# Performance work log

Hardware: AMD Instinct MI355X
Metric: run time of the kernel (lower is better)

Reference implementation:

```python
import jax, jax.numpy as jnp
import numpy as np

H, D, K, FF = 4, 256, 1024, 1024  # n_head, d_model, key_feature_dim, dim_feedforward
L, B = 2048, 4                    # pixels, batch


def setup_inputs() -> dict:
    key = jax.random.key(0)
    ks = jax.random.split(key, 12)
    def g(k, shape, s=0.02):
        return jax.random.normal(k, shape, jnp.float32) * s
    return dict(
        src=jax.random.normal(ks[0], (L, B, D), jnp.float32),
        WK=g(ks[1], (H, K, D), (2.0 / K) ** 0.5),
        WQ=g(ks[2], (H, K, D), (2.0 / K) ** 0.5),
        WV=g(ks[3], (H, D, D), (2.0 / D) ** 0.5),
        TC=g(ks[4], (H, D, D)),
        ENw1=g(ks[5], (H, FF, D)), ENb1=jnp.zeros((H, FF), jnp.float32),
        ENw2=g(ks[6], (H, D, FF)), ENb2=jnp.zeros((H, D), jnp.float32),
        ENg=jnp.ones((H, D), jnp.float32), ENbeta=jnp.zeros((H, D), jnp.float32),
        Wout=g(ks[7], (D, H * D)),
        L1w=g(ks[8], (FF, D)), L1b=jnp.zeros((FF,), jnp.float32),
        L2w=g(ks[9], (D, FF)), L2b=jnp.zeros((D,), jnp.float32),
        N1g=jnp.ones((D,), jnp.float32), N1b=jnp.zeros((D,), jnp.float32),
        N2g=jnp.ones((D,), jnp.float32), N2b=jnp.zeros((D,), jnp.float32),
    )


def _ln(x, g, b, eps=1e-5):
    m = jnp.mean(x, -1, keepdims=True)
    v = jnp.mean((x - m) ** 2, -1, keepdims=True)
    return (x - m) * jax.lax.rsqrt(v + eps) * g + b


def _l2n(x, eps=1e-12):
    n = jnp.sqrt(jnp.sum(x * x, -1, keepdims=True))
    return x / jnp.maximum(n, eps)


def reference(src, WK, WQ, WV, TC, ENw1, ENb1, ENw2, ENb2, ENg, ENbeta,
              Wout, L1w, L1b, L2w, L2b, N1g, N1b, N2g, N2b):
    # --- RMA: per-head RelationUnit, vectorized over head axis h ---
    wq = _l2n(jnp.einsum('lbd,hkd->hlbk', src, WQ))   # (H,L,B,K), L2-normed
    wk = _l2n(jnp.einsum('lbd,hkd->hlbk', src, WK))
    wv = jnp.einsum('lbd,hed->hlbe', src, WV)         # (H,L,B,D)
    dot = jnp.einsum('hlbk,hmbk->hblm', wq, wk)       # (H,B,Lq,Lk)
    aff = jax.nn.softmax(dot, axis=-1)                 # softmax over keys (temp=1)
    aff = aff / (1e-9 + jnp.sum(aff, axis=2, keepdims=True))  # renorm over QUERY dim (torch dim=1)
    out = jnp.einsum('hblm,hmbe->hlbe', aff, wv)       # (H,L,B,D)
    ru = jax.nn.relu(jnp.einsum('hlbe,hfe->hlbf', src[None] - out, TC))
    # per-head extra TransNonlinear: residual MLP + layernorm
    hid = jax.nn.relu(jnp.einsum('hlbd,hfd->hlbf', ru, ENw1) + ENb1[:, None, None, :])
    s2 = jnp.einsum('hlbf,hdf->hlbd', hid, ENw2) + ENb2[:, None, None, :]
    tn = _ln(ru + s2, ENg[:, None, None, :], ENbeta[:, None, None, :])  # (H,L,B,D)
    concat = jnp.transpose(tn, (1, 2, 0, 3)).reshape(L, B, H * D)
    attn = concat @ Wout.T                              # (L,B,D)
    # --- encoder layer: residual + LN + FFN + LN (dropout = eval identity) ---
    x = _ln(src + attn, N1g, N1b)
    ff = jax.nn.relu(x @ L1w.T + L1b) @ L2w.T + L2b
    return _ln(x + ff, N2g, N2b)
```

## Files before the change

### kernel.cpp

```cpp
#include <hip/hip_runtime.h>
#include <hip/hip_bf16.h>

typedef __hip_bfloat16 bf16;
typedef short s16x8 __attribute__((ext_vector_type(8)));
typedef float f32x4 __attribute__((ext_vector_type(4)));

#ifndef __has_builtin
#define __has_builtin(x) 0
#endif
#if __has_builtin(__builtin_amdgcn_global_load_lds)
#define HAS_GLL 1
#else
#define HAS_GLL 0
#endif

#define HN 4
#define DM 256
#define KF 1024
#define FFD 1024
#define LL 2048
#define BB 4
#define NN (LL * BB)
#define HD (HN * DM)

__device__ __forceinline__ float b2f(unsigned short u) {
    unsigned v = ((unsigned)u) << 16; float f; __builtin_memcpy(&f, &v, 4); return f;
}
__device__ __forceinline__ unsigned short f2b(float f) {
    bf16 b = (bf16)f; unsigned short u; __builtin_memcpy(&u, &b, 2); return u;
}

__device__ __forceinline__ float waveReduceSum(float v) {
    for (int o = 32; o; o >>= 1) v += __shfl_down(v, o, 64);
    return v;
}
__device__ __forceinline__ float waveReduceMax(float v) {
    for (int o = 32; o; o >>= 1) v = fmaxf(v, __shfl_down(v, o, 64));
    return v;
}
__device__ __forceinline__ float blockReduceSum(float v) {
    __shared__ float sh[4];
    v = waveReduceSum(v);
    __syncthreads();
    if ((threadIdx.x & 63) == 0) sh[threadIdx.x >> 6] = v;
    __syncthreads();
    return sh[0] + sh[1] + sh[2] + sh[3];
}
__device__ __forceinline__ float blockReduceMax(float v) {
    __shared__ float sh[4];
    v = waveReduceMax(v);
    __syncthreads();
    if ((threadIdx.x & 63) == 0) sh[threadIdx.x >> 6] = v;
    __syncthreads();
    return fmaxf(fmaxf(sh[0], sh[1]), fmaxf(sh[2], sh[3]));
}

__global__ void sentinel_kernel(float* out, float val) {
    if (threadIdx.x == 0 && blockIdx.x == 0) out[0] = val;
}

#if HAS_GLL
__device__ __forceinline__ void gll16(void* g, void* l) {
    __builtin_amdgcn_global_load_lds(
        (__attribute__((address_space(1))) unsigned int*)g,
        (__attribute__((address_space(3))) unsigned int*)l, 16, 0, 0);
}
#endif

__global__ __launch_bounds__(256) void gemm_nt(
    const void* __restrict__ A, int aF32, int lda, long sA,
    const void* __restrict__ Bv, int bF32, int ldb, long sB,
    void* __restrict__ C, int cF32, int ldc, long sC,
    int Kc,
    const float* __restrict__ bias, long sBias,
    const void* __restrict__ aux, int auxType, int ldaux, long sAux,
    float accSign, int relu)
{
    const int z = blockIdx.z;
    const float* Af = (const float*)A + (long)z * sA;
    const bf16*  Ah = (const bf16*)A + (long)z * sA;
    const float* Bf = (const float*)Bv + (long)z * sB;
    const bf16*  Bh = (const bf16*)Bv + (long)z * sB;
    float* Cf = (float*)C + (long)z * sC;
    bf16*  Ch = (bf16*)C + (long)z * sC;
    const float* biasp = bias ? (bias + (long)z * sBias) : nullptr;
    const float* auxf = (auxType == 1) ? ((const float*)aux + (long)z * sAux) : nullptr;
    const bf16*  auxh = (auxType == 2) ? ((const bf16*)aux + (long)z * sAux) : nullptr;

    __shared__ __align__(16) bf16 As[128 * 32];
    __shared__ __align__(16) bf16 Bs[128 * 32];

    const int tid = threadIdx.x;
    const int lane = tid & 63;
    const int wv = __builtin_amdgcn_readfirstlane(tid >> 6);
    const int wm = (tid >> 6) & 1;
    const int wn = (tid >> 6) >> 1;
    const int lrow = lane & 15;
    const int quad = lane >> 4;
    const int m0 = blockIdx.x * 128;
    const int n0 = blockIdx.y * 128;
    const int srow = tid >> 1;
    const int scol = (tid & 1) * 16;
    const int drow = wv * 16 + (lane >> 2);
    const int dcol = (lane & 3) * 8;

    f32x4 acc[4][4] = {};

    for (int k0 = 0; k0 < Kc; k0 += 32) {
        uint4 av0, av1, bv0, bv1;
        if (aF32) {
            const float* ag = Af + (long)(m0 + srow) * lda + k0 + scol;
            ushort t[16];
#pragma unroll
            for (int j = 0; j < 4; j++) {
                float4 f = *(const float4*)(ag + 4 * j);
                t[4*j] = f2b(f.x); t[4*j+1] = f2b(f.y); t[4*j+2] = f2b(f.z); t[4*j+3] = f2b(f.w);
            }
            av0 = *(const uint4*)&t[0]; av1 = *(const uint4*)&t[8];
        }
#if !HAS_GLL
        else {
            const bf16* ag = Ah + (long)(m0 + srow) * lda + k0 + scol;
            av0 = *(const uint4*)ag; av1 = *(const uint4*)(ag + 8);
        }
#endif
        if (bF32) {
            const float* bg = Bf + (long)(n0 + srow) * ldb + k0 + scol;
            ushort t[16];
#pragma unroll
            for (int j = 0; j < 4; j++) {
                float4 f = *(const float4*)(bg + 4 * j);
                t[4*j] = f2b(f.x); t[4*j+1] = f2b(f.y); t[4*j+2] = f2b(f.z); t[4*j+3] = f2b(f.w);
            }
            bv0 = *(const uint4*)&t[0]; bv1 = *(const uint4*)&t[8];
        }
#if !HAS_GLL
        else {
            const bf16* bg = Bh + (long)(n0 + srow) * ldb + k0 + scol;
            bv0 = *(const uint4*)bg; bv1 = *(const uint4*)(bg + 8);
        }
#endif
        __syncthreads();
        if (aF32) {
            *(uint4*)&As[srow * 32 + scol] = av0;
            *(uint4*)&As[srow * 32 + scol + 8] = av1;
        } else {
#if HAS_GLL
            gll16((void*)(Ah + (long)(m0 + drow) * lda + k0 + dcol), (void*)(As + wv * 512));
            gll16((void*)(Ah + (long)(m0 + 64 + drow) * lda + k0 + dcol), (void*)(As + 2048 + wv * 512));
#else
            *(uint4*)&As[srow * 32 + scol] = av0;
            *(uint4*)&As[srow * 32 + scol + 8] = av1;
#endif
        }
        if (bF32) {
            *(uint4*)&Bs[srow * 32 + scol] = bv0;
            *(uint4*)&Bs[srow * 32 + scol + 8] = bv1;
        } else {
#if HAS_GLL
            gll16((void*)(Bh + (long)(n0 + drow) * ldb + k0 + dcol), (void*)(Bs + wv * 512));
            gll16((void*)(Bh + (long)(n0 + 64 + drow) * ldb + k0 + dcol), (void*)(Bs + 2048 + wv * 512));
#else
            *(uint4*)&Bs[srow * 32 + scol] = bv0;
            *(uint4*)&Bs[srow * 32 + scol + 8] = bv1;
#endif
        }
        __syncthreads();

        s16x8 af[4], bfg[4];
#pragma unroll
        for (int mi = 0; mi < 4; mi++) {
            int r = wm * 64 + mi * 16 + lrow;
            af[mi] = *(const s16x8*)&As[r * 32 + quad * 8];
        }
#pragma unroll
        for (int ni = 0; ni < 4; ni++) {
            int r = wn * 64 + ni * 16 + lrow;
            bfg[ni] = *(const s16x8*)&Bs[r * 32 + quad * 8];
        }
#pragma unroll
        for (int mi = 0; mi < 4; mi++)
#pragma unroll
            for (int ni = 0; ni < 4; ni++)
                acc[mi][ni] = __builtin_amdgcn_mfma_f32_16x16x32_bf16(af[mi], bfg[ni], acc[mi][ni], 0, 0, 0);
    }

#pragma unroll
    for (int mi = 0; mi < 4; mi++) {
#pragma unroll
        for (int ni = 0; ni < 4; ni++) {
            int col = n0 + wn * 64 + ni * 16 + lrow;
            float bv = biasp ? biasp[col] : 0.0f;
#pragma unroll
            for (int i = 0; i < 4; i++) {
                int row = m0 + wm * 64 + mi * 16 + quad * 4 + i;
                float v = accSign * acc[mi][ni][i] + bv;
                if (auxType == 1) v += auxf[(long)row * ldaux + col];
                else if (auxType == 2) v += (float)auxh[(long)row * ldaux + col];
                if (relu) v = fmaxf(v, 0.0f);
                if (cF32) Cf[(long)row * ldc + col] = v;
                else Ch[(long)row * ldc + col] = (bf16)v;
            }
        }
    }
}

__global__ __launch_bounds__(256) void cvt4(const float* __restrict__ in, bf16* __restrict__ out, int n4) {
    int i = blockIdx.x * 256 + threadIdx.x;
    if (i < n4) {
        float4 f = ((const float4*)in)[i];
        ushort4 u; u.x = f2b(f.x); u.y = f2b(f.y); u.z = f2b(f.z); u.w = f2b(f.w);
        ((ushort4*)out)[i] = u;
    }
}

struct WCvt {
    const float* in[9];
    bf16* out[9];
    int n4[9];
};
__global__ __launch_bounds__(256) void cvt_weights(WCvt wc) {
    int t = blockIdx.y;
    int n4 = wc.n4[t];
    const float4* in = (const float4*)wc.in[t];
    ushort4* out = (ushort4*)wc.out[t];
    for (int i = blockIdx.x * 256 + threadIdx.x; i < n4; i += gridDim.x * 256) {
        float4 f = in[i];
        ushort4 u; u.x = f2b(f.x); u.y = f2b(f.y); u.z = f2b(f.z); u.w = f2b(f.w);
        out[i] = u;
    }
}

__global__ __launch_bounds__(256) void l2norm_rows(bf16* __restrict__ Q) {
    bf16* q = Q + (long)blockIdx.x * KF;
    ushort4 u = ((ushort4*)q)[threadIdx.x];
    float v0 = b2f(u.x), v1 = b2f(u.y), v2 = b2f(u.z), v3 = b2f(u.w);
    float ss = blockReduceSum(v0 * v0 + v1 * v1 + v2 * v2 + v3 * v3);
    float inv = 1.0f / fmaxf(sqrtf(ss), 1e-12f);
    u.x = f2b(v0 * inv); u.y = f2b(v1 * inv); u.z = f2b(v2 * inv); u.w = f2b(v3 * inv);
    ((ushort4*)q)[threadIdx.x] = u;
}

__global__ __launch_bounds__(256) void softmax_rows(bf16* __restrict__ P) {
    bf16* p = P + (long)blockIdx.x * LL;
    ushort4 a = ((ushort4*)p)[2 * threadIdx.x];
    ushort4 b = ((ushort4*)p)[2 * threadIdx.x + 1];
    float v[8] = {b2f(a.x), b2f(a.y), b2f(a.z), b2f(a.w), b2f(b.x), b2f(b.y), b2f(b.z), b2f(b.w)};
    float mx = -1e30f;
#pragma unroll
    for (int i = 0; i < 8; i++) mx = fmaxf(mx, v[i]);
    mx = blockReduceMax(mx);
    float s = 0.0f;
#pragma unroll
    for (int i = 0; i < 8; i++) { v[i] = __expf(v[i] - mx); s += v[i]; }
    s = blockReduceSum(s);
    float inv = 1.0f / s;
    a.x = f2b(v[0]*inv); a.y = f2b(v[1]*inv); a.z = f2b(v[2]*inv); a.w = f2b(v[3]*inv);
    b.x = f2b(v[4]*inv); b.y = f2b(v[5]*inv); b.z = f2b(v[6]*inv); b.w = f2b(v[7]*inv);
    ((ushort4*)p)[2 * threadIdx.x] = a;
    ((ushort4*)p)[2 * threadIdx.x + 1] = b;
}

__global__ __launch_bounds__(256) void zero_cs(float* __restrict__ cs) {
    cs[blockIdx.x * 256 + threadIdx.x] = 0.0f;
}

__global__ __launch_bounds__(256) void colsum2(const bf16* __restrict__ P, float* __restrict__ cs) {
    int col = blockIdx.x * 256 + threadIdx.x;
    int rc = blockIdx.y;
    int b = blockIdx.z;
    const bf16* p = P + (long)b * LL * LL + (long)rc * 128 * LL + col;
    float s = 0.0f;
#pragma unroll 4
    for (int r = 0; r < 128; r++) s += (float)p[(long)r * LL];
    atomicAdd(&cs[(long)b * LL + col], s);
}

__global__ __launch_bounds__(256) void scale_vt(bf16* __restrict__ vt, const float* __restrict__ cs) {
    int e = blockIdx.x, b = blockIdx.y;
    bf16* row = vt + ((long)b * DM + e) * LL;
    const float* c = cs + (long)b * LL;
#pragma unroll
    for (int i = 0; i < 8; i++) {
        int m = threadIdx.x + i * 256;
        row[m] = (bf16)((float)row[m] / (1e-9f + c[m]));
    }
}

__global__ __launch_bounds__(256) void ln_rows(const bf16* __restrict__ in, void* __restrict__ out,
                                               int outF32,
                                               const float* __restrict__ g, const float* __restrict__ b,
                                               const float* __restrict__ aux) {
    long base = (long)blockIdx.x * 256;
    float v = (float)in[base + threadIdx.x];
    if (aux) v += aux[base + threadIdx.x];
    float mean = blockReduceSum(v) * (1.0f / 256.0f);
    float d = v - mean;
    float var = blockReduceSum(d * d) * (1.0f / 256.0f);
    float o = d * rsqrtf(var + 1e-5f) * g[threadIdx.x] + b[threadIdx.x];
    if (outF32) ((float*)out)[base + threadIdx.x] = o;
    else ((bf16*)out)[base + threadIdx.x] = (bf16)o;
}

__global__ __launch_bounds__(256) void ln_cat(bf16* __restrict__ cat, const float* __restrict__ g,
                                              const float* __restrict__ bb) {
    long n = blockIdx.x;
    int h = blockIdx.y;
    bf16* x = cat + n * HD + (long)h * DM;
    float v = (float)x[threadIdx.x];
    float mean = blockReduceSum(v) * (1.0f / 256.0f);
    float d = v - mean;
    float var = blockReduceSum(d * d) * (1.0f / 256.0f);
    x[threadIdx.x] = (bf16)(d * rsqrtf(var + 1e-5f) * g[h * DM + threadIdx.x] + bb[h * DM + threadIdx.x]);
}

extern "C" void kernel_launch(void* const* d_in, const int* in_sizes, int n_in,
                              void* d_out, int out_size, void* d_ws, size_t ws_size,
                              hipStream_t stream) {
    const float* src  = (const float*)d_in[0];
    const float* WK   = (const float*)d_in[1];
    const float* WQ   = (const float*)d_in[2];
    const float* WV   = (const float*)d_in[3];
    const float* TC   = (const float*)d_in[4];
    const float* ENw1 = (const float*)d_in[5];
    const float* ENb1 = (const float*)d_in[6];
    const float* ENw2 = (const float*)d_in[7];
    const float* ENb2 = (const float*)d_in[8];
    const float* ENg  = (const float*)d_in[9];
    const float* ENbt = (const float*)d_in[10];
    const float* Wout = (const float*)d_in[11];
    const float* L1w  = (const float*)d_in[12];
    const float* L1b  = (const float*)d_in[13];
    const float* L2w  = (const float*)d_in[14];
    const float* L2b  = (const float*)d_in[15];
    const float* N1g  = (const float*)d_in[16];
    const float* N1b  = (const float*)d_in[17];
    const float* N2g  = (const float*)d_in[18];
    const float* N2b  = (const float*)d_in[19];

    const size_t COMPACT_FLOOR = 34700000;
    const size_t FAST_FLOOR  = 92307456;
    const size_t FASTW_FLOOR = 92307456 + 11010048;
    if (ws_size < COMPACT_FLOOR || out_size != NN * DM || n_in != 20) {
        float val;
        if (n_in != 20) val = 32768.0f + (float)n_in;
        else if (out_size != NN * DM) val = 49152.0f;
        else val = 16384.0f + 128.0f * (float)(unsigned)(ws_size >> 20);
        sentinel_kernel<<<1, 64, 0, stream>>>((float*)d_out, val);
        return;
    }

    char* w = (char*)d_ws;
    auto G = [&](const void* A, int aF, int lda, long sA,
                 const void* B, int bF, int ldb, long sB,
                 void* C, int cF, int ldc, long sC,
                 int M, int Nn, int Kc, int nb,
                 const float* bias, long sBias,
                 const void* aux, int auxT, int ldaux, long sAux,
                 float sgn, int relu) {
        gemm_nt<<<dim3(M / 128, Nn / 128, nb), dim3(256), 0, stream>>>(
            A, aF, lda, sA, B, bF, ldb, sB, C, cF, ldc, sC, Kc,
            bias, sBias, aux, auxT, ldaux, sAux, sgn, relu);
    };

    if (ws_size >= FAST_FLOOR) {
        bf16*  Sb  = (bf16*)(w + 0);
        bf16*  Q   = (bf16*)(w + 4194304);
        bf16*  K   = (bf16*)(w + 20971520);
        bf16*  Vt  = (bf16*)(w + 37748736);
        bf16*  P   = (bf16*)(w + 41943040);
        bf16*  Su  = (bf16*)(w + 75497472);
        float* Cs  = (float*)(w + 92274688);
        bf16* Ru = Q; bf16* Hid = K; bf16* Cat = P;
        bf16* Attn = Vt; bf16* Xln = Su; bf16* Ffh = Q; bf16* Yp = Vt;

        const int haveWb = (ws_size >= FASTW_FLOOR) ? 1 : 0;
        char* wb = w + 92307456;
        bf16* WKb   = (bf16*)(wb + 0);
        bf16* WQb   = (bf16*)(wb + 2097152);
        bf16* WVb   = (bf16*)(wb + 4194304);
        bf16* TCb   = (bf16*)(wb + 4718592);
        bf16* ENw1b = (bf16*)(wb + 5242880);
        bf16* ENw2b = (bf16*)(wb + 7340032);
        bf16* Woutb = (bf16*)(wb + 9437184);
        bf16* L1wb  = (bf16*)(wb + 9961472);
        bf16* L2wb  = (bf16*)(wb + 10485760);
        if (haveWb) {
            WCvt wc;
            wc.in[0] = WK;   wc.out[0] = WKb;   wc.n4[0] = 262144;
            wc.in[1] = WQ;   wc.out[1] = WQb;   wc.n4[1] = 262144;
            wc.in[2] = WV;   wc.out[2] = WVb;   wc.n4[2] = 65536;
            wc.in[3] = TC;   wc.out[3] = TCb;   wc.n4[3] = 65536;
            wc.in[4] = ENw1; wc.out[4] = ENw1b; wc.n4[4] = 262144;
            wc.in[5] = ENw2; wc.out[5] = ENw2b; wc.n4[5] = 262144;
            wc.in[6] = Wout; wc.out[6] = Woutb; wc.n4[6] = 65536;
            wc.in[7] = L1w;  wc.out[7] = L1wb;  wc.n4[7] = 65536;
            wc.in[8] = L2w;  wc.out[8] = L2wb;  wc.n4[8] = 65536;
            cvt_weights<<<dim3(256, 9), 256, 0, stream>>>(wc);
        }
        const int wF = haveWb ? 0 : 1;
        auto WP = [&](const void* f32p, const void* b16p, long off) {
            return haveWb ? (const void*)((const bf16*)b16p + off)
                          : (const void*)((const float*)f32p + off);
        };

        cvt4<<<2048, 256, 0, stream>>>(src, Sb, NN * DM / 4);

        for (int h = 0; h < HN; h++) {
            G(Sb, 0, DM, 0, WP(WQ, WQb, (long)h * KF * DM), wF, DM, 0, Q, 0, KF, 0,
              NN, KF, DM, 1, nullptr, 0, nullptr, 0, 0, 0, 1.0f, 0);
            G(Sb, 0, DM, 0, WP(WK, WKb, (long)h * KF * DM), wF, DM, 0, K, 0, KF, 0,
              NN, KF, DM, 1, nullptr, 0, nullptr, 0, 0, 0, 1.0f, 0);
            G(WP(WV, WVb, (long)h * DM * DM), wF, DM, 0, Sb, 0, BB * DM, DM,
              Vt, 0, LL, (long)DM * LL,
              DM, LL, DM, BB, nullptr, 0, nullptr, 0, 0, 0, 1.0f, 0);
            l2norm_rows<<<NN, 256, 0, stream>>>(Q);
            l2norm_rows<<<NN, 256, 0, stream>>>(K);
            G(Q, 0, BB * KF, KF, K, 0, BB * KF, KF, P, 0, LL, (long)LL * LL,
              LL, LL, KF, BB, nullptr, 0, nullptr, 0, 0, 0, 1.0f, 0);
            softmax_rows<<<BB * LL, 256, 0, stream>>>(P);
            zero_cs<<<BB * LL / 256, 256, 0, stream>>>(Cs);
            colsum2<<<dim3(LL / 256, 16, BB), 256, 0, stream>>>(P, Cs);
            scale_vt<<<dim3(DM, BB), 256, 0, stream>>>(Vt, Cs);
            G(P, 0, LL, (long)LL * LL, Vt, 0, LL, (long)DM * LL,
              Su + (long)h * NN * DM, 0, BB * DM, DM,
              LL, DM, LL, BB, nullptr, 0, Sb, 2, BB * DM, DM, -1.0f, 0);
        }
        G(Su, 0, DM, (long)NN * DM, WP(TC, TCb, 0), wF, DM, (long)DM * DM,
          Ru, 0, DM, (long)NN * DM,
          NN, DM, DM, HN, nullptr, 0, nullptr, 0, 0, 0, 1.0f, 1);
        for (int h = 0; h < HN; h++) {
            G(Ru + (long)h * NN * DM, 0, DM, 0, WP(ENw1, ENw1b, (long)h * FFD * DM), wF, DM, 0,
              Hid, 0, FFD, 0, NN, FFD, DM, 1, ENb1 + (long)h * FFD, 0, nullptr, 0, 0, 0, 1.0f, 1);
            G(Hid, 0, FFD, 0, WP(ENw2, ENw2b, (long)h * DM * FFD), wF, FFD, 0,
              Cat + (long)h * DM, 0, HD, 0, NN, DM, FFD, 1,
              ENb2 + (long)h * DM, 0, Ru + (long)h * NN * DM, 2, DM, 0, 1.0f, 0);
        }
        ln_cat<<<dim3(NN, HN), 256, 0, stream>>>(Cat, ENg, ENbt);
        G(Cat, 0, HD, 0, WP(Wout, Woutb, 0), wF, HD, 0, Attn, 0, DM, 0,
          NN, DM, HD, 1, nullptr, 0, nullptr, 0, 0, 0, 1.0f, 0);
        ln_rows<<<NN, 256, 0, stream>>>(Attn, Xln, 0, N1g, N1b, src);
        G(Xln, 0, DM, 0, WP(L1w, L1wb, 0), wF, DM, 0, Ffh, 0, FFD, 0,
          NN, FFD, DM, 1, L1b, 0, nullptr, 0, 0, 0, 1.0f, 1);
        G(Ffh, 0, FFD, 0, WP(L2w, L2wb, 0), wF, FFD, 0, Yp, 0, DM, 0,
          NN, DM, FFD, 1, L2b, 0, Xln, 2, DM, 0, 1.0f, 0);
        ln_rows<<<NN, 256, 0, stream>>>(Yp, (float*)d_out, 1, N2g, N2b, nullptr);
    } else {
        bf16*  S0 = (bf16*)(w + 0);
        bf16*  S1 = (bf16*)(w + 16777216);
        bf16*  S2 = (bf16*)(w + 20971520);
        bf16*  S3 = (bf16*)(w + 25165824);
        bf16*  S4 = (bf16*)(w + 26214400);
        bf16*  S5 = (bf16*)(w + 30408704);
        float* Cs = (float*)(w + 34603008);

        for (int h = 0; h < HN; h++) {
            for (int b = 0; b < BB; b++) {
                G(src + b * DM, 1, BB * DM, 0, WQ + (long)h * KF * DM, 1, DM, 0,
                  S1, 0, KF, 0, LL, KF, DM, 1, nullptr, 0, nullptr, 0, 0, 0, 1.0f, 0);
                G(src + b * DM, 1, BB * DM, 0, WK + (long)h * KF * DM, 1, DM, 0,
                  S2, 0, KF, 0, LL, KF, DM, 1, nullptr, 0, nullptr, 0, 0, 0, 1.0f, 0);
                G(WV + (long)h * DM * DM, 1, DM, 0, src + b * DM, 1, BB * DM, 0,
                  S3, 0, LL, 0, DM, LL, DM, 1, nullptr, 0, nullptr, 0, 0, 0, 1.0f, 0);
                l2norm_rows<<<LL, 256, 0, stream>>>(S1);
                l2norm_rows<<<LL, 256, 0, stream>>>(S2);
                G(S1, 0, KF, 0, S2, 0, KF, 0, S0, 0, LL, 0,
                  LL, LL, KF, 1, nullptr, 0, nullptr, 0, 0, 0, 1.0f, 0);
                softmax_rows<<<LL, 256, 0, stream>>>(S0);
                zero_cs<<<LL / 256, 256, 0, stream>>>(Cs);
                colsum2<<<dim3(LL / 256, 16, 1), 256, 0, stream>>>(S0, Cs);
                scale_vt<<<dim3(DM, 1), 256, 0, stream>>>(S3, Cs);
                G(S0, 0, LL, 0, S3, 0, LL, 0, S4 + b * DM, 0, BB * DM, 0,
                  LL, DM, LL, 1, nullptr, 0, src + b * DM, 1, BB * DM, 0, -1.0f, 0);
            }
            G(S4, 0, DM, 0, TC + (long)h * DM * DM, 1, DM, 0, S1, 0, DM, 0,
              NN, DM, DM, 1, nullptr, 0, nullptr, 0, 0, 0, 1.0f, 1);
            G(S1, 0, DM, 0, ENw1 + (long)h * FFD * DM, 1, DM, 0, S0, 0, FFD, 0,
              NN, FFD, DM, 1, ENb1 + (long)h * FFD, 0, nullptr, 0, 0, 0, 1.0f, 1);
            G(S0, 0, FFD, 0, ENw2 + (long)h * DM * FFD, 1, FFD, 0, S2, 0, DM, 0,
              NN, DM, FFD, 1, ENb2 + (long)h * DM, 0, S1, 2, DM, 0, 1.0f, 0);
            ln_rows<<<NN, 256, 0, stream>>>(S2, S2, 0, ENg + (long)h * DM, ENbt + (long)h * DM, nullptr);
            G(S2, 0, DM, 0, Wout + (long)h * DM, 1, HD, 0, S5, 0, DM, 0,
              NN, DM, DM, 1, nullptr, 0, (h == 0) ? nullptr : (const void*)S5,
              (h == 0) ? 0 : 2, DM, 0, 1.0f, 0);
        }
        ln_rows<<<NN, 256, 0, stream>>>(S5, S1, 0, N1g, N1b, src);
        G(S1, 0, DM, 0, L1w, 1, DM, 0, S0, 0, FFD, 0,
          NN, FFD, DM, 1, L1b, 0, nullptr, 0, 0, 0, 1.0f, 1);
        G(S0, 0, FFD, 0, L2w, 1, FFD, 0, S2, 0, DM, 0,
          NN, DM, FFD, 1, L2b, 0, S1, 2, DM, 0, 1.0f, 0);
        ln_rows<<<NN, 256, 0, stream>>>(S2, (float*)d_out, 1, N2g, N2b, nullptr);
    }
}
```

Before: 1.282 ms.

## Double-buffer GEMM LDS staging and add BN=64 tile variant for narrow GEMMs

```diff
diff --git a/kernel.cpp b/kernel.cpp
--- a/kernel.cpp
+++ b/kernel.cpp
@@ -67,6 +67,7 @@
 }
 #endif
 
+template<int BN>
 __global__ __launch_bounds__(256) void gemm_nt(
     const void* __restrict__ A, int aF32, int lda, long sA,
     const void* __restrict__ Bv, int bF32, int ldb, long sB,
@@ -76,6 +77,8 @@
     const void* __restrict__ aux, int auxType, int ldaux, long sAux,
     float accSign, int relu)
 {
+    constexpr int NI = BN / 32;
+    constexpr int WN = BN / 2;
     const int z = blockIdx.z;
     const float* Af = (const float*)A + (long)z * sA;
     const bf16*  Ah = (const bf16*)A + (long)z * sA;
@@ -87,8 +90,8 @@
     const float* auxf = (auxType == 1) ? ((const float*)aux + (long)z * sAux) : nullptr;
     const bf16*  auxh = (auxType == 2) ? ((const bf16*)aux + (long)z * sAux) : nullptr;
 
-    __shared__ __align__(16) bf16 As[128 * 32];
-    __shared__ __align__(16) bf16 Bs[128 * 32];
+    __shared__ __align__(16) bf16 As[2][128 * 32];
+    __shared__ __align__(16) bf16 Bs[2][BN * 32];
 
     const int tid = threadIdx.x;
     const int lane = tid & 63;
@@ -98,103 +101,144 @@
     const int lrow = lane & 15;
     const int quad = lane >> 4;
     const int m0 = blockIdx.x * 128;
-    const int n0 = blockIdx.y * 128;
+    const int n0 = blockIdx.y * BN;
     const int srow = tid >> 1;
     const int scol = (tid & 1) * 16;
     const int drow = wv * 16 + (lane >> 2);
     const int dcol = (lane & 3) * 8;
 
-    f32x4 acc[4][4] = {};
-
-    for (int k0 = 0; k0 < Kc; k0 += 32) {
-        uint4 av0, av1, bv0, bv1;
-        if (aF32) {
-            const float* ag = Af + (long)(m0 + srow) * lda + k0 + scol;
-            ushort t[16];
-#pragma unroll
-            for (int j = 0; j < 4; j++) {
-                float4 f = *(const float4*)(ag + 4 * j);
-                t[4*j] = f2b(f.x); t[4*j+1] = f2b(f.y); t[4*j+2] = f2b(f.z); t[4*j+3] = f2b(f.w);
-            }
-            av0 = *(const uint4*)&t[0]; av1 = *(const uint4*)&t[8];
-        }
+    f32x4 acc[4][NI] = {};
+
+#if HAS_GLL
+    if (!aF32 && !bF32) {
+        const int nk = Kc >> 5;
+        auto stage = [&](int k0, int buf) {
+            const bf16* a0 = Ah + (long)(m0 + drow) * lda + k0 + dcol;
+            gll16((void*)a0, (void*)&As[buf][wv * 512]);
+            gll16((void*)(a0 + (long)lda * 64), (void*)&As[buf][2048 + wv * 512]);
+            const bf16* b0 = Bh + (long)(n0 + drow) * ldb + k0 + dcol;
+            gll16((void*)b0, (void*)&Bs[buf][wv * 512]);
+            if (BN == 128)
+                gll16((void*)(b0 + (long)ldb * 64), (void*)&Bs[buf][2048 + wv * 512]);
+        };
+        stage(0, 0);
+        __syncthreads();
+        int cur = 0;
+        for (int t = 0; t < nk; ++t) {
+            if (t + 1 < nk) stage((t + 1) << 5, cur ^ 1);
+            s16x8 af[4], bfg[NI];
+#pragma unroll
+            for (int mi = 0; mi < 4; mi++)
+                af[mi] = *(const s16x8*)&As[cur][(wm * 64 + mi * 16 + lrow) * 32 + quad * 8];
+#pragma unroll
+            for (int ni = 0; ni < NI; ni++)
+                bfg[ni] = *(const s16x8*)&Bs[cur][(wn * WN + ni * 16 + lrow) * 32 + quad * 8];
+#pragma unroll
+            for (int mi = 0; mi < 4; mi++)
+#pragma unroll
+                for (int ni = 0; ni < NI; ni++)
+                    acc[mi][ni] = __builtin_amdgcn_mfma_f32_16x16x32_bf16(af[mi], bfg[ni], acc[mi][ni], 0, 0, 0);
+            __syncthreads();
+            cur ^= 1;
+        }
+    } else
+#endif
+    {
+        for (int k0 = 0; k0 < Kc; k0 += 32) {
+            uint4 av0, av1, bv0, bv1;
+            if (aF32) {
+                const float* ag = Af + (long)(m0 + srow) * lda + k0 + scol;
+                ushort t[16];
+#pragma unroll
+                for (int j = 0; j < 4; j++) {
+                    float4 f = *(const float4*)(ag + 4 * j);
+                    t[4*j] = f2b(f.x); t[4*j+1] = f2b(f.y); t[4*j+2] = f2b(f.z); t[4*j+3] = f2b(f.w);
+                }
+                av0 = *(const uint4*)&t[0]; av1 = *(const uint4*)&t[8];
+            }
 #if !HAS_GLL
-        else {
-            const bf16* ag = Ah + (long)(m0 + srow) * lda + k0 + scol;
-            av0 = *(const uint4*)ag; av1 = *(const uint4*)(ag + 8);
-        }
-#endif
-        if (bF32) {
-            const float* bg = Bf + (long)(n0 + srow) * ldb + k0 + scol;
-            ushort t[16];
-#pragma unroll
-            for (int j = 0; j < 4; j++) {
-                float4 f = *(const float4*)(bg + 4 * j);
-                t[4*j] = f2b(f.x); t[4*j+1] = f2b(f.y); t[4*j+2] = f2b(f.z); t[4*j+3] = f2b(f.w);
-            }
-            bv0 = *(const uint4*)&t[0]; bv1 = *(const uint4*)&t[8];
-        }
+            else {
+                const bf16* ag = Ah + (long)(m0 + srow) * lda + k0 + scol;
+                av0 = *(const uint4*)ag; av1 = *(const uint4*)(ag + 8);
+            }
+#endif
+            if (bF32) {
+                if (srow < BN) {
+                    const float* bg = Bf + (long)(n0 + srow) * ldb + k0 + scol;
+                    ushort t[16];
+#pragma unroll
+                    for (int j = 0; j < 4; j++) {
+                        float4 f = *(const float4*)(bg + 4 * j);
+                        t[4*j] = f2b(f.x); t[4*j+1] = f2b(f.y); t[4*j+2] = f2b(f.z); t[4*j+3] = f2b(f.w);
+                    }
+                    bv0 = *(const uint4*)&t[0]; bv1 = *(const uint4*)&t[8];
+                }
+            }
 #if !HAS_GLL
-        else {
-            const bf16* bg = Bh + (long)(n0 + srow) * ldb + k0 + scol;
-            bv0 = *(const uint4*)bg; bv1 = *(const uint4*)(bg + 8);
-        }
-#endif
-        __syncthreads();
-        if (aF32) {
-            *(uint4*)&As[srow * 32 + scol] = av0;
-            *(uint4*)&As[srow * 32 + scol + 8] = av1;
-        } else {
+            else {
+                if (srow < BN) {
+                    const bf16* bg = Bh + (long)(n0 + srow) * ldb + k0 + scol;
+                    bv0 = *(const uint4*)bg; bv1 = *(const uint4*)(bg + 8);
+                }
+            }
+#endif
+            __syncthreads();
+            if (aF32) {
+                *(uint4*)&As[0][srow * 32 + scol] = av0;
+                *(uint4*)&As[0][srow * 32 + scol + 8] = av1;
+            } else {
 #if HAS_GLL
-            gll16((void*)(Ah + (long)(m0 + drow) * lda + k0 + dcol), (void*)(As + wv * 512));
-            gll16((void*)(Ah + (long)(m0 + 64 + drow) * lda + k0 + dcol), (void*)(As + 2048 + wv * 512));
+                gll16((void*)(Ah + (long)(m0 + drow) * lda + k0 + dcol), (void*)&As[0][wv * 512]);
+                gll16((void*)(Ah + (long)(m0 + 64 + drow) * lda + k0 + dcol), (void*)&As[0][2048 + wv * 512]);
 #else
-            *(uint4*)&As[srow * 32 + scol] = av0;
-            *(uint4*)&As[srow * 32 + scol + 8] = av1;
-#endif
-        }
-        if (bF32) {
-            *(uint4*)&Bs[srow * 32 + scol] = bv0;
-            *(uint4*)&Bs[srow * 32 + scol + 8] = bv1;
-        } else {
+                *(uint4*)&As[0][srow * 32 + scol] = av0;
+                *(uint4*)&As[0][srow * 32 + scol + 8] = av1;
+#endif
+            }
+            if (bF32) {
+                if (srow < BN) {
+                    *(uint4*)&Bs[0][srow * 32 + scol] = bv0;
+                    *(uint4*)&Bs[0][srow * 32 + scol + 8] = bv1;
+                }
+            } else {
 #if HAS_GLL
-            gll16((void*)(Bh + (long)(n0 + drow) * ldb + k0 + dcol), (void*)(Bs + wv * 512));
-            gll16((void*)(Bh + (long)(n0 + 64 + drow) * ldb + k0 + dcol), (void*)(Bs + 2048 + wv * 512));
+                gll16((void*)(Bh + (long)(n0 + drow) * ldb + k0 + dcol), (void*)&Bs[0][wv * 512]);
+                if (BN == 128)
+                    gll16((void*)(Bh + (long)(n0 + 64 + drow) * ldb + k0 + dcol), (void*)&Bs[0][2048 + wv * 512]);
 #else
-            *(uint4*)&Bs[srow * 32 + scol] = bv0;
-            *(uint4*)&Bs[srow * 32 + scol + 8] = bv1;
-#endif
-        }
-        __syncthreads();
-
-        s16x8 af[4], bfg[4];
-#pragma unroll
-        for (int mi = 0; mi < 4; mi++) {
-            int r = wm * 64 + mi * 16 + lrow;
-            af[mi] = *(const s16x8*)&As[r * 32 + quad * 8];
-        }
-#pragma unroll
-        for (int ni = 0; ni < 4; ni++) {
-            int r = wn * 64 + ni * 16 + lrow;
-            bfg[ni] = *(const s16x8*)&Bs[r * 32 + quad * 8];
-        }
-#pragma unroll
-        for (int mi = 0; mi < 4; mi++)
-#pragma unroll
-            for (int ni = 0; ni < 4; ni++)
-                acc[mi][ni] = __builtin_amdgcn_mfma_f32_16x16x32_bf16(af[mi], bfg[ni], acc[mi][ni], 0, 0, 0);
+                if (srow < BN) {
+                    *(uint4*)&Bs[0][srow * 32 + scol] = bv0;
+                    *(uint4*)&Bs[0][srow * 32 + scol + 8] = bv1;
+                }
+#endif
+            }
+            __syncthreads();
+
+            s16x8 af[4], bfg[NI];
+#pragma unroll
+            for (int mi = 0; mi < 4; mi++)
+                af[mi] = *(const s16x8*)&As[0][(wm * 64 + mi * 16 + lrow) * 32 + quad * 8];
+#pragma unroll
+            for (int ni = 0; ni < NI; ni++)
+                bfg[ni] = *(const s16x8*)&Bs[0][(wn * WN + ni * 16 + lrow) * 32 + quad * 8];
+#pragma unroll
+            for (int mi = 0; mi < 4; mi++)
+#pragma unroll
+                for (int ni = 0; ni < NI; ni++)
+                    acc[mi][ni] = __builtin_amdgcn_mfma_f32_16x16x32_bf16(af[mi], bfg[ni], acc[mi][ni], 0, 0, 0);
+        }
     }
 
 #pragma unroll
     for (int mi = 0; mi < 4; mi++) {
 #pragma unroll
-        for (int ni = 0; ni < 4; ni++) {
-            int col = n0 + wn * 64 + ni * 16 + lrow;
-            float bv = biasp ? biasp[col] : 0.0f;
+        for (int ni = 0; ni < NI; ni++) {
+            int col = n0 + wn * WN + ni * 16 + lrow;
+            float bvl = biasp ? biasp[col] : 0.0f;
 #pragma unroll
             for (int i = 0; i < 4; i++) {
                 int row = m0 + wm * 64 + mi * 16 + quad * 4 + i;
-                float v = accSign * acc[mi][ni][i] + bv;
+                float v = accSign * acc[mi][ni][i] + bvl;
                 if (auxType == 1) v += auxf[(long)row * ldaux + col];
                 else if (auxType == 2) v += (float)auxh[(long)row * ldaux + col];
                 if (relu) v = fmaxf(v, 0.0f);
@@ -358,7 +402,18 @@
                  const float* bias, long sBias,
                  const void* aux, int auxT, int ldaux, long sAux,
                  float sgn, int relu) {
-        gemm_nt<<<dim3(M / 128, Nn / 128, nb), dim3(256), 0, stream>>>(
+        gemm_nt<128><<<dim3(M / 128, Nn / 128, nb), dim3(256), 0, stream>>>(
+            A, aF, lda, sA, B, bF, ldb, sB, C, cF, ldc, sC, Kc,
+            bias, sBias, aux, auxT, ldaux, sAux, sgn, relu);
+    };
+    auto G64 = [&](const void* A, int aF, int lda, long sA,
+                 const void* B, int bF, int ldb, long sB,
+                 void* C, int cF, int ldc, long sC,
+                 int M, int Nn, int Kc, int nb,
+                 const float* bias, long sBias,
+                 const void* aux, int auxT, int ldaux, long sAux,
+                 float sgn, int relu) {
+        gemm_nt<64><<<dim3(M / 128, Nn / 64, nb), dim3(256), 0, stream>>>(
             A, aF, lda, sA, B, bF, ldb, sB, C, cF, ldc, sC, Kc,
             bias, sBias, aux, auxT, ldaux, sAux, sgn, relu);
     };
@@ -411,7 +466,7 @@
               NN, KF, DM, 1, nullptr, 0, nullptr, 0, 0, 0, 1.0f, 0);
             G(Sb, 0, DM, 0, WP(WK, WKb, (long)h * KF * DM), wF, DM, 0, K, 0, KF, 0,
               NN, KF, DM, 1, nullptr, 0, nullptr, 0, 0, 0, 1.0f, 0);
-            G(WP(WV, WVb, (long)h * DM * DM), wF, DM, 0, Sb, 0, BB * DM, DM,
+            G64(WP(WV, WVb, (long)h * DM * DM), wF, DM, 0, Sb, 0, BB * DM, DM,
               Vt, 0, LL, (long)DM * LL,
               DM, LL, DM, BB, nullptr, 0, nullptr, 0, 0, 0, 1.0f, 0);
             l2norm_rows<<<NN, 256, 0, stream>>>(Q);
@@ -422,7 +477,7 @@
             zero_cs<<<BB * LL / 256, 256, 0, stream>>>(Cs);
             colsum2<<<dim3(LL / 256, 16, BB), 256, 0, stream>>>(P, Cs);
             scale_vt<<<dim3(DM, BB), 256, 0, stream>>>(Vt, Cs);
-            G(P, 0, LL, (long)LL * LL, Vt, 0, LL, (long)DM * LL,
+            G64(P, 0, LL, (long)LL * LL, Vt, 0, LL, (long)DM * LL,
               Su + (long)h * NN * DM, 0, BB * DM, DM,
               LL, DM, LL, BB, nullptr, 0, Sb, 2, BB * DM, DM, -1.0f, 0);
         }
@@ -432,17 +487,17 @@
         for (int h = 0; h < HN; h++) {
             G(Ru + (long)h * NN * DM, 0, DM, 0, WP(ENw1, ENw1b, (long)h * FFD * DM), wF, DM, 0,
               Hid, 0, FFD, 0, NN, FFD, DM, 1, ENb1 + (long)h * FFD, 0, nullptr, 0, 0, 0, 1.0f, 1);
-            G(Hid, 0, FFD, 0, WP(ENw2, ENw2b, (long)h * DM * FFD), wF, FFD, 0,
+            G64(Hid, 0, FFD, 0, WP(ENw2, ENw2b, (long)h * DM * FFD), wF, FFD, 0,
               Cat + (long)h * DM, 0, HD, 0, NN, DM, FFD, 1,
               ENb2 + (long)h * DM, 0, Ru + (long)h * NN * DM, 2, DM, 0, 1.0f, 0);
         }
         ln_cat<<<dim3(NN, HN), 256, 0, stream>>>(Cat, ENg, ENbt);
-        G(Cat, 0, HD, 0, WP(Wout, Woutb, 0), wF, HD, 0, Attn, 0, DM, 0,
+        G64(Cat, 0, HD, 0, WP(Wout, Woutb, 0), wF, HD, 0, Attn, 0, DM, 0,
           NN, DM, HD, 1, nullptr, 0, nullptr, 0, 0, 0, 1.0f, 0);
         ln_rows<<<NN, 256, 0, stream>>>(Attn, Xln, 0, N1g, N1b, src);
         G(Xln, 0, DM, 0, WP(L1w, L1wb, 0), wF, DM, 0, Ffh, 0, FFD, 0,
           NN, FFD, DM, 1, L1b, 0, nullptr, 0, 0, 0, 1.0f, 1);
-        G(Ffh, 0, FFD, 0, WP(L2w, L2wb, 0), wF, FFD, 0, Yp, 0, DM, 0,
+        G64(Ffh, 0, FFD, 0, WP(L2w, L2wb, 0), wF, FFD, 0, Yp, 0, DM, 0,
           NN, DM, FFD, 1, L2b, 0, Xln, 2, DM, 0, 1.0f, 0);
         ln_rows<<<NN, 256, 0, stream>>>(Yp, (float*)d_out, 1, N2g, N2b, nullptr);
     } else {
```

Measured after the change: 1.140 ms. -11.1%, faster.
